# Performance work log

Hardware: AMD Instinct MI355X
Metric: run time of the kernel (lower is better)

## Reference

```python
import jax, jax.numpy as jnp
import numpy as np

N, E = 50000, 800000
IN_CH, OUT_CH = 128, 16
H1, D1 = 2, 2 * OUT_CH           # conv1: heads=2, per-head dim 32, concat -> 64
MID = H1 * D1                    # 64
NEG_SLOPE = 0.2

def setup_inputs() -> dict:
    key = jax.random.key(0)
    ks = jax.random.split(key, 16)
    s = lambda k, shape: jax.random.normal(k, shape, dtype=jnp.float32) * 0.1
    return {
        "x": jax.random.normal(ks[0], (N, IN_CH), dtype=jnp.float32),
        "edge_index": jax.random.randint(ks[1], (2, E), 0, N, dtype=jnp.int64),
        "W1": s(ks[2], (IN_CH, H1 * D1)),
        "att_src1": s(ks[3], (H1, D1)),
        "att_dst1": s(ks[4], (H1, D1)),
        "b1": jnp.zeros((MID,), jnp.float32),
        "W_mu": s(ks[5], (MID, OUT_CH)),
        "att_src_mu": s(ks[6], (1, OUT_CH)),
        "att_dst_mu": s(ks[7], (1, OUT_CH)),
        "b_mu": jnp.zeros((OUT_CH,), jnp.float32),
        "W_ls": s(ks[8], (MID, OUT_CH)),
        "att_src_ls": s(ks[9], (1, OUT_CH)),
        "att_dst_ls": s(ks[10], (1, OUT_CH)),
        "b_ls": jnp.zeros((OUT_CH,), jnp.float32),
    }

def gat_conv(x, src, dst, W, att_src, att_dst, bias, heads, d):
    # x: [N, F]; src/dst: [E'] (self loops included); PyG GATConv, eval mode (dropout off)
    n = x.shape[0]
    h = (x @ W).reshape(n, heads, d)                     # [N, H, D]
    a_src = jnp.sum(h * att_src, axis=-1)                # [N, H]
    a_dst = jnp.sum(h * att_dst, axis=-1)                # [N, H]
    e = jax.nn.leaky_relu(a_src[src] + a_dst[dst], NEG_SLOPE)   # [E', H]
    # segment softmax over incoming edges of each destination node
    m = jax.ops.segment_max(e, dst, num_segments=n)
    ex = jnp.exp(e - m[dst])
    denom = jax.ops.segment_sum(ex, dst, num_segments=n)
    alpha = ex / (denom[dst] + 1e-16)                    # [E', H]
    msg = h[src] * alpha[:, :, None]                     # [E', H, D]
    out = jax.ops.segment_sum(msg, dst, num_segments=n)  # [N, H, D]
    return out, bias

def reference(x, edge_index, W1, att_src1, att_dst1, b1,
              W_mu, att_src_mu, att_dst_mu, b_mu,
              W_ls, att_src_ls, att_dst_ls, b_ls):
    n = x.shape[0]
    loops = jnp.arange(n, dtype=edge_index.dtype)
    src = jnp.concatenate([edge_index[0], loops])        # add_self_loops=True (inputs have none)
    dst = jnp.concatenate([edge_index[1], loops])
    h, b = gat_conv(x, src, dst, W1, att_src1, att_dst1, b1, H1, D1)
    h = jax.nn.relu(h.reshape(n, H1 * D1) + b)           # concat=True -> [N, 64]
    mu, bm = gat_conv(h, src, dst, W_mu, att_src_mu, att_dst_mu, b_mu, 1, OUT_CH)
    ls, bl = gat_conv(h, src, dst, W_ls, att_src_ls, att_dst_ls, b_ls, 1, OUT_CH)
    mu = mu.mean(axis=1) + bm                            # concat=False, heads=1 -> mean == squeeze
    ls = ls.mean(axis=1) + bl
    return (mu, ls)
```

## Files before the change

### kernel.cpp

```cpp
#include <hip/hip_runtime.h>

#define NEG 0.2f

typedef __attribute__((ext_vector_type(8))) short short8;
typedef __attribute__((ext_vector_type(4))) float f32x4;

__device__ __forceinline__ float lrelu(float v) { return v > 0.f ? v : NEG * v; }

__device__ __forceinline__ unsigned short f2bf(float f) {
    unsigned u = __float_as_uint(f);
    unsigned r = (u + 0x7FFF + ((u >> 16) & 1)) >> 16;
    return (unsigned short)r;
}
__device__ __forceinline__ float bf2f(unsigned short h) { return __uint_as_float((unsigned)h << 16); }
__device__ __forceinline__ float bf_lo(unsigned v) { return __uint_as_float(v << 16); }
__device__ __forceinline__ float bf_hi(unsigned v) { return __uint_as_float(v & 0xffff0000u); }

__global__ void build_w(const float* __restrict__ W1, const float* __restrict__ as1,
                        const float* __restrict__ ad1,
                        const float* __restrict__ Wmu, const float* __restrict__ Wls,
                        const float* __restrict__ asmu, const float* __restrict__ admu,
                        const float* __restrict__ asls, const float* __restrict__ adls,
                        unsigned short* __restrict__ w1h, unsigned short* __restrict__ w1l,
                        unsigned short* __restrict__ w2h, unsigned short* __restrict__ w2l) {
    int i = blockIdx.x * blockDim.x + threadIdx.x;
    if (i < 128 * 80) {
        int k = i / 80, c = i % 80;
        float val;
        if (c < 64) val = W1[k * 64 + c];
        else if (c < 68) {
            int j = c - 64;
            int hh = j & 1;
            const float* att = (j >= 2) ? ad1 : as1;
            float s = 0.f;
            for (int d = 0; d < 32; ++d) s += W1[k * 64 + hh * 32 + d] * att[hh * 32 + d];
            val = s;
        } else val = 0.f;
        unsigned short h = f2bf(val);
        w1h[c * 128 + k] = h;
        w1l[c * 128 + k] = f2bf(val - bf2f(h));
    } else {
        int i2 = i - 128 * 80;
        if (i2 >= 64 * 48) return;
        int k = i2 / 48, c = i2 % 48;
        float val;
        if (c < 16) val = Wmu[k * 16 + c];
        else if (c < 32) val = Wls[k * 16 + (c - 16)];
        else if (c < 36) {
            int j = c - 32;
            const float* W = (j < 2) ? Wmu : Wls;
            const float* att = (j == 0) ? asmu : (j == 1) ? admu : (j == 2) ? asls : adls;
            float s = 0.f;
            for (int c2 = 0; c2 < 16; ++c2) s += W[k * 16 + c2] * att[c2];
            val = s;
        } else val = 0.f;
        unsigned short h = f2bf(val);
        w2h[c * 64 + k] = h;
        w2l[c * 64 + k] = f2bf(val - bf2f(h));
    }
}

__global__ __launch_bounds__(256) void gemm1(const float* __restrict__ x,
                                             const unsigned short* __restrict__ Wt_hi,
                                             const unsigned short* __restrict__ Wt_lo,
                                             unsigned short* __restrict__ hbf,
                                             float* __restrict__ a1, float2* __restrict__ a1s, int n) {
    int wid = threadIdx.x >> 6, lane = threadIdx.x & 63;
    int m = lane & 15, b = lane >> 4;
    int row = blockIdx.x * 64 + wid * 16 + m;
    int rowc = min(row, n - 1);
    short8 ah[4], al[4];
    const float* xp = x + (size_t)rowc * 128 + b * 8;
#pragma unroll
    for (int kc = 0; kc < 4; ++kc) {
        float4 v0 = *(const float4*)(xp + kc * 32);
        float4 v1 = *(const float4*)(xp + kc * 32 + 4);
        float vv[8] = {v0.x, v0.y, v0.z, v0.w, v1.x, v1.y, v1.z, v1.w};
#pragma unroll
        for (int j = 0; j < 8; ++j) {
            unsigned short h = f2bf(vv[j]);
            ah[kc][j] = (short)h;
            al[kc][j] = (short)f2bf(vv[j] - bf2f(h));
        }
    }
    int orow0 = blockIdx.x * 64 + wid * 16 + b * 4;
#pragma unroll
    for (int ct = 0; ct < 5; ++ct) {
        f32x4 acc = {0.f, 0.f, 0.f, 0.f};
        int col = ct * 16 + m;
        const unsigned short* wh = Wt_hi + col * 128 + b * 8;
        const unsigned short* wl = Wt_lo + col * 128 + b * 8;
#pragma unroll
        for (int kc = 0; kc < 4; ++kc) {
            short8 bh = *(const short8*)(wh + kc * 32);
            short8 bl = *(const short8*)(wl + kc * 32);
            acc = __builtin_amdgcn_mfma_f32_16x16x32_bf16(ah[kc], bh, acc, 0, 0, 0);
            acc = __builtin_amdgcn_mfma_f32_16x16x32_bf16(al[kc], bh, acc, 0, 0, 0);
            acc = __builtin_amdgcn_mfma_f32_16x16x32_bf16(ah[kc], bl, acc, 0, 0, 0);
        }
        if (ct < 4) {
#pragma unroll
            for (int j = 0; j < 4; ++j) {
                int orow = orow0 + j;
                if (orow < n) hbf[(size_t)orow * 64 + ct * 16 + m] = f2bf(acc[j]);
            }
        } else {
            int base = lane & 48;
#pragma unroll
            for (int j = 0; j < 4; ++j) {
                float c0 = __shfl(acc[j], base + 0, 64);
                float c1 = __shfl(acc[j], base + 1, 64);
                int orow = orow0 + j;
                if (orow < n) {
                    if (m < 4) a1[(size_t)orow * 4 + m] = acc[j];
                    if (m == 0) a1s[orow] = make_float2(c0, c1);
                }
            }
        }
    }
}

__global__ __launch_bounds__(256) void gemm2(const unsigned short* __restrict__ h1bf,
                                             const unsigned short* __restrict__ Wt_hi,
                                             const unsigned short* __restrict__ Wt_lo,
                                             unsigned* __restrict__ hml, float* __restrict__ a2,
                                             float2* __restrict__ a2s, int n) {
    int wid = threadIdx.x >> 6, lane = threadIdx.x & 63;
    int m = lane & 15, b = lane >> 4;
    int row = blockIdx.x * 64 + wid * 16 + m;
    int rowc = min(row, n - 1);
    short8 a0 = *(const short8*)(h1bf + (size_t)rowc * 64 + b * 8);
    short8 a1f = *(const short8*)(h1bf + (size_t)rowc * 64 + 32 + b * 8);
    int orow0 = blockIdx.x * 64 + wid * 16 + b * 4;
    f32x4 accs[3];
#pragma unroll
    for (int ct = 0; ct < 3; ++ct) {
        f32x4 acc = {0.f, 0.f, 0.f, 0.f};
        int col = ct * 16 + m;
        const unsigned short* wh = Wt_hi + col * 64 + b * 8;
        const unsigned short* wl = Wt_lo + col * 64 + b * 8;
        short8 bh0 = *(const short8*)(wh);
        short8 bl0 = *(const short8*)(wl);
        short8 bh1 = *(const short8*)(wh + 32);
        short8 bl1 = *(const short8*)(wl + 32);
        acc = __builtin_amdgcn_mfma_f32_16x16x32_bf16(a0, bh0, acc, 0, 0, 0);
        acc = __builtin_amdgcn_mfma_f32_16x16x32_bf16(a0, bl0, acc, 0, 0, 0);
        acc = __builtin_amdgcn_mfma_f32_16x16x32_bf16(a1f, bh1, acc, 0, 0, 0);
        acc = __builtin_amdgcn_mfma_f32_16x16x32_bf16(a1f, bl1, acc, 0, 0, 0);
        accs[ct] = acc;
    }
    int base = lane & 48;
#pragma unroll
    for (int j = 0; j < 4; ++j) {
        int orow = orow0 + j;
        float c0 = __shfl(accs[2][j], base + 0, 64);
        float c2 = __shfl(accs[2][j], base + 2, 64);
        if (orow >= n) continue;
        hml[(size_t)orow * 16 + m] = ((unsigned)f2bf(accs[1][j]) << 16) | f2bf(accs[0][j]);
        if (m < 4) a2[(size_t)orow * 4 + m] = accs[2][j];
        if (m == 0) a2s[orow] = make_float2(c0, c2);
    }
}

__global__ __launch_bounds__(256) void count_deg_part(const int* __restrict__ dstv, int E, int np,
                                                      int* __restrict__ deg) {
    int p = blockIdx.x & 7;
    int bslot = blockIdx.x >> 3;
    int nblk = gridDim.x >> 3;
    int lo = p * np, hi = lo + np;
    for (int i = bslot * 256 + threadIdx.x; i < E; i += nblk * 256) {
        int d = dstv[i];
        if (d >= lo && d < hi) atomicAdd(&deg[d], 1);
    }
}

__global__ __launch_bounds__(256) void scatter_part(const int* __restrict__ srcv,
                                                    const int* __restrict__ dstv, int E, int np,
                                                    int* __restrict__ cursor, int* __restrict__ srcs) {
    int p = blockIdx.x & 7;
    int bslot = blockIdx.x >> 3;
    int nblk = gridDim.x >> 3;
    int lo = p * np, hi = lo + np;
    for (int i = bslot * 256 + threadIdx.x; i < E; i += nblk * 256) {
        int d = dstv[i];
        if (d >= lo && d < hi) {
            int slot = atomicAdd(&cursor[d], 1);
            srcs[slot] = srcv[i];
        }
    }
}

__global__ __launch_bounds__(256) void block_sums(const int* __restrict__ deg, int n,
                                                  int* __restrict__ bsums) {
    int i = blockIdx.x * 256 + threadIdx.x;
    int v = (i < n) ? deg[i] : 0;
    for (int o = 32; o > 0; o >>= 1) v += __shfl_down(v, o, 64);
    __shared__ int ws[4];
    if ((threadIdx.x & 63) == 0) ws[threadIdx.x >> 6] = v;
    __syncthreads();
    if (threadIdx.x == 0) bsums[blockIdx.x] = ws[0] + ws[1] + ws[2] + ws[3];
}

__global__ __launch_bounds__(256) void write_offs(const int* __restrict__ deg,
                                                  const int* __restrict__ bsums, int nb, int n,
                                                  int* __restrict__ offs, int* __restrict__ cursor) {
    __shared__ int sb[256];
    __shared__ int s[256];
    int t = threadIdx.x;
    int bv = (t < nb) ? bsums[t] : 0;
    sb[t] = bv;
    __syncthreads();
    for (int o = 1; o < 256; o <<= 1) {
        int u = (t >= o) ? sb[t - o] : 0;
        __syncthreads();
        sb[t] += u;
        __syncthreads();
    }
    int base0 = (blockIdx.x == 0) ? 0 : sb[blockIdx.x - 1];
    int i = blockIdx.x * 256 + t;
    int v = (i < n) ? deg[i] : 0;
    s[t] = v;
    __syncthreads();
    for (int o = 1; o < 256; o <<= 1) {
        int u = (t >= o) ? s[t - o] : 0;
        __syncthreads();
        s[t] += u;
        __syncthreads();
    }
    int excl = s[t] - v + base0;
    if (i < n) { offs[i] = excl; cursor[i] = excl; }
    if (i == n - 1) offs[n] = excl + v;
}

__global__ __launch_bounds__(256) void agg1(const unsigned* __restrict__ h32, const float* __restrict__ a1,
                                            const float2* __restrict__ a1s,
                                            const int* __restrict__ offs, const int* __restrict__ srcs,
                                            const float* __restrict__ b1, unsigned* __restrict__ h1u, int n) {
    int wid = threadIdx.x >> 6, lane = threadIdx.x & 63;
    int node = blockIdx.x * 4 + wid;
    if (node >= n) return;
    int q = lane >> 4;
    int l = lane & 15;
    int head = l >> 3;
    float adst = a1[node * 4 + 2 + head];
    float ax = 0.f, ay = 0.f, az = 0.f, aw = 0.f, denom = 0.f;
    if (q == 0) {
        float w = __expf(lrelu(a1[node * 4 + head] + adst));
        uint2 hv = *(const uint2*)&h32[node * 32 + 2 * l];
        ax = w * bf_lo(hv.x); ay = w * bf_hi(hv.x);
        az = w * bf_lo(hv.y); aw = w * bf_hi(hv.y);
        denom = w;
    }
    int kb = offs[node];
    int deg = offs[node + 1] - kb;
    int pre = (lane < deg) ? srcs[kb + lane] : 0;
    for (int idx0 = 0; idx0 < deg; idx0 += 4) {
        int idx = idx0 + q;
        int idc = min(idx, deg - 1);
        int s = (idc < 64) ? __shfl(pre, idc, 64) : srcs[kb + idc];
        float2 ap = a1s[s];
        float asrc = head ? ap.y : ap.x;
        float wv = (idx < deg) ? __expf(lrelu(asrc + adst)) : 0.f;
        uint2 hv = *(const uint2*)&h32[s * 32 + 2 * l];
        denom += wv;
        ax += wv * bf_lo(hv.x); ay += wv * bf_hi(hv.x);
        az += wv * bf_lo(hv.y); aw += wv * bf_hi(hv.y);
    }
    ax += __shfl_xor(ax, 16, 64); ax += __shfl_xor(ax, 32, 64);
    ay += __shfl_xor(ay, 16, 64); ay += __shfl_xor(ay, 32, 64);
    az += __shfl_xor(az, 16, 64); az += __shfl_xor(az, 32, 64);
    aw += __shfl_xor(aw, 16, 64); aw += __shfl_xor(aw, 32, 64);
    denom += __shfl_xor(denom, 16, 64); denom += __shfl_xor(denom, 32, 64);
    if (q == 0) {
        float4 bv = *(const float4*)&b1[4 * l];
        float o0 = fmaxf(ax / denom + bv.x, 0.f);
        float o1 = fmaxf(ay / denom + bv.y, 0.f);
        float o2 = fmaxf(az / denom + bv.z, 0.f);
        float o3 = fmaxf(aw / denom + bv.w, 0.f);
        uint2 o;
        o.x = ((unsigned)f2bf(o1) << 16) | f2bf(o0);
        o.y = ((unsigned)f2bf(o3) << 16) | f2bf(o2);
        *(uint2*)&h1u[node * 32 + 2 * l] = o;
    }
}

__global__ __launch_bounds__(256) void agg2(const unsigned* __restrict__ hml,
                                            const float* __restrict__ a2, const float2* __restrict__ a2s,
                                            const int* __restrict__ offs, const int* __restrict__ srcs,
                                            const float* __restrict__ bmu, const float* __restrict__ bls,
                                            float* __restrict__ out, int n) {
    int wid = threadIdx.x >> 6, lane = threadIdx.x & 63;
    int node = blockIdx.x * 4 + wid;
    if (node >= n) return;
    int q = lane >> 4, c = lane & 15;
    float admu = a2[node * 4 + 1], adls = a2[node * 4 + 3];
    float amu = 0.f, als = 0.f, dmu = 0.f, dls = 0.f;
    if (q == 0) {
        float wmu = __expf(lrelu(a2[node * 4 + 0] + admu));
        float wls = __expf(lrelu(a2[node * 4 + 2] + adls));
        unsigned hv = hml[node * 16 + c];
        amu = wmu * bf_lo(hv); als = wls * bf_hi(hv);
        dmu = wmu; dls = wls;
    }
    int kb = offs[node];
    int deg = offs[node + 1] - kb;
    int pre = (lane < deg) ? srcs[kb + lane] : 0;
    for (int idx0 = 0; idx0 < deg; idx0 += 4) {
        int idx = idx0 + q;
        int idc = min(idx, deg - 1);
        int s = (idc < 64) ? __shfl(pre, idc, 64) : srcs[kb + idc];
        float2 ap = a2s[s];
        bool ok = idx < deg;
        float w1v = ok ? __expf(lrelu(ap.x + admu)) : 0.f;
        float w2v = ok ? __expf(lrelu(ap.y + adls)) : 0.f;
        unsigned hv = hml[s * 16 + c];
        dmu += w1v; dls += w2v;
        amu += w1v * bf_lo(hv);
        als += w2v * bf_hi(hv);
    }
    amu += __shfl_xor(amu, 16, 64); amu += __shfl_xor(amu, 32, 64);
    als += __shfl_xor(als, 16, 64); als += __shfl_xor(als, 32, 64);
    dmu += __shfl_xor(dmu, 16, 64); dmu += __shfl_xor(dmu, 32, 64);
    dls += __shfl_xor(dls, 16, 64); dls += __shfl_xor(dls, 32, 64);
    if (q == 0) {
        out[node * 16 + c] = amu / dmu + bmu[c];
        out[(size_t)n * 16 + node * 16 + c] = als / dls + bls[c];
    }
}

extern "C" void kernel_launch(void* const* d_in, const int* in_sizes, int n_in,
                              void* d_out, int out_size, void* d_ws, size_t ws_size,
                              hipStream_t stream) {
    const float* x    = (const float*)d_in[0];
    const int*   ei   = (const int*)d_in[1];
    const float* W1   = (const float*)d_in[2];
    const float* as1  = (const float*)d_in[3];
    const float* ad1  = (const float*)d_in[4];
    const float* b1   = (const float*)d_in[5];
    const float* Wmu  = (const float*)d_in[6];
    const float* asmu = (const float*)d_in[7];
    const float* admu = (const float*)d_in[8];
    const float* bmu  = (const float*)d_in[9];
    const float* Wls  = (const float*)d_in[10];
    const float* asls = (const float*)d_in[11];
    const float* adls = (const float*)d_in[12];
    const float* bls  = (const float*)d_in[13];
    float* out = (float*)d_out;

    int n = in_sizes[0] / 128;
    int E = in_sizes[1] / 2;
    int np = (n + 7) / 8;

    char* ws = (char*)d_ws;
    size_t off = 0;
    auto alloc = [&](size_t b) { size_t p = off; off = (off + b + 255) & ~(size_t)255; return p; };

    unsigned short* hbf  = (unsigned short*)(ws + alloc((size_t)n * 64 * 2));
    unsigned*       h1u  = (unsigned*)(ws + alloc((size_t)n * 32 * 4));
    float*          a1   = (float*)(ws + alloc((size_t)n * 4 * 4));
    float2*         a1s  = (float2*)(ws + alloc((size_t)n * 8));
    unsigned*       hml  = (unsigned*)(ws + alloc((size_t)n * 16 * 4));
    float*          a2   = (float*)(ws + alloc((size_t)n * 4 * 4));
    float2*         a2s  = (float2*)(ws + alloc((size_t)n * 8));
    unsigned short* w1h  = (unsigned short*)(ws + alloc(80 * 128 * 2));
    unsigned short* w1l  = (unsigned short*)(ws + alloc(80 * 128 * 2));
    unsigned short* w2h  = (unsigned short*)(ws + alloc(48 * 64 * 2));
    unsigned short* w2l  = (unsigned short*)(ws + alloc(48 * 64 * 2));
    int*   deg    = (int*)(ws + alloc((size_t)n * 4));
    int*   offs   = (int*)(ws + alloc((size_t)(n + 1) * 4));
    int*   cursor = (int*)(ws + alloc((size_t)n * 4));
    int*   srcs   = (int*)(ws + alloc((size_t)E * 4));
    int*   bsums  = (int*)(ws + alloc(1024 * 4));

    int nb = (n + 255) / 256;

    hipMemsetAsync(deg, 0, (size_t)n * 4, stream);
    build_w<<<(128 * 80 + 64 * 48 + 255) / 256, 256, 0, stream>>>(W1, as1, ad1, Wmu, Wls, asmu, admu,
                                                                  asls, adls, w1h, w1l, w2h, w2l);
    gemm1<<<(n + 63) / 64, 256, 0, stream>>>(x, w1h, w1l, hbf, a1, a1s, n);
    count_deg_part<<<2048, 256, 0, stream>>>(ei + E, E, np, deg);
    block_sums<<<nb, 256, 0, stream>>>(deg, n, bsums);
    write_offs<<<nb, 256, 0, stream>>>(deg, bsums, nb, n, offs, cursor);
    scatter_part<<<2048, 256, 0, stream>>>(ei, ei + E, E, np, cursor, srcs);
    agg1<<<(n + 3) / 4, 256, 0, stream>>>((const unsigned*)hbf, a1, a1s, offs, srcs, b1, h1u, n);
    gemm2<<<(n + 63) / 64, 256, 0, stream>>>((const unsigned short*)h1u, w2h, w2l, hml, a2, a2s, n);
    agg2<<<(n + 3) / 4, 256, 0, stream>>>(hml, a2, a2s, offs, srcs, bmu, bls, out, n);
}
```

Measured before the change: 284.2 us.

## Pre-bin edges by destination partition before degree counting and CSR scatter

Adds a bin_edges pass that buckets (src,dst) pairs into 8 destination partitions using a shared-memory histogram. Degree counting and scatter then read only their own partition instead of each of 8 block groups scanning and filtering the whole edge list. The aggregation loops also drop the shuffle-based prefetch of source indices and load srcs directly with a strided loop. This costs an extra pairs buffer and one pass writing 8-byte pairs, and relies on each partition's count staying under a fixed capacity (E/8+8192), which could overflow on skewed graphs.

```diff
diff --git a/kernel.cpp b/kernel.cpp
--- a/kernel.cpp
+++ b/kernel.cpp
@@ -162,31 +162,56 @@
     }
 }
 
-__global__ __launch_bounds__(256) void count_deg_part(const int* __restrict__ dstv, int E, int np,
-                                                      int* __restrict__ deg) {
+__global__ __launch_bounds__(256) void bin_edges(const int* __restrict__ srcv,
+                                                 const int* __restrict__ dstv, int E, int np, int cap,
+                                                 int* __restrict__ pcnt, int2* __restrict__ pairs) {
+    __shared__ int hist[8], base[8], cur[8];
+    int t = threadIdx.x;
+    if (t < 8) { hist[t] = 0; cur[t] = 0; }
+    __syncthreads();
+    int e0 = blockIdx.x * 1024;
+    int e1 = min(e0 + 1024, E);
+    int d[4], se[4];
+    int cnt = 0;
+    for (int e = e0 + t; e < e1; e += 256) {
+        int dd = dstv[e];
+        d[cnt] = dd; se[cnt] = e; ++cnt;
+        atomicAdd(&hist[(unsigned)dd / (unsigned)np], 1);
+    }
+    __syncthreads();
+    if (t < 8) base[t] = atomicAdd(&pcnt[t], hist[t]);
+    __syncthreads();
+    for (int j = 0; j < cnt; ++j) {
+        int p = (unsigned)d[j] / (unsigned)np;
+        int slot = atomicAdd(&cur[p], 1);
+        pairs[(size_t)p * cap + base[p] + slot] = make_int2(srcv[se[j]], d[j]);
+    }
+}
+
+__global__ __launch_bounds__(256) void count_pairs(const int2* __restrict__ pairs,
+                                                   const int* __restrict__ pcnt, int cap,
+                                                   int* __restrict__ deg) {
     int p = blockIdx.x & 7;
     int bslot = blockIdx.x >> 3;
     int nblk = gridDim.x >> 3;
-    int lo = p * np, hi = lo + np;
-    for (int i = bslot * 256 + threadIdx.x; i < E; i += nblk * 256) {
-        int d = dstv[i];
-        if (d >= lo && d < hi) atomicAdd(&deg[d], 1);
-    }
-}
-
-__global__ __launch_bounds__(256) void scatter_part(const int* __restrict__ srcv,
-                                                    const int* __restrict__ dstv, int E, int np,
-                                                    int* __restrict__ cursor, int* __restrict__ srcs) {
+    int cnt = pcnt[p];
+    const int2* pp = pairs + (size_t)p * cap;
+    for (int i = bslot * 256 + threadIdx.x; i < cnt; i += nblk * 256)
+        atomicAdd(&deg[pp[i].y], 1);
+}
+
+__global__ __launch_bounds__(256) void scatter_pairs(const int2* __restrict__ pairs,
+                                                     const int* __restrict__ pcnt, int cap,
+                                                     int* __restrict__ cursor, int* __restrict__ srcs) {
     int p = blockIdx.x & 7;
     int bslot = blockIdx.x >> 3;
     int nblk = gridDim.x >> 3;
-    int lo = p * np, hi = lo + np;
-    for (int i = bslot * 256 + threadIdx.x; i < E; i += nblk * 256) {
-        int d = dstv[i];
-        if (d >= lo && d < hi) {
-            int slot = atomicAdd(&cursor[d], 1);
-            srcs[slot] = srcv[i];
-        }
+    int cnt = pcnt[p];
+    const int2* pp = pairs + (size_t)p * cap;
+    for (int i = bslot * 256 + threadIdx.x; i < cnt; i += nblk * 256) {
+        int2 e = pp[i];
+        int slot = atomicAdd(&cursor[e.y], 1);
+        srcs[slot] = e.x;
     }
 }
 
@@ -251,16 +276,12 @@
         az = w * bf_lo(hv.y); aw = w * bf_hi(hv.y);
         denom = w;
     }
-    int kb = offs[node];
-    int deg = offs[node + 1] - kb;
-    int pre = (lane < deg) ? srcs[kb + lane] : 0;
-    for (int idx0 = 0; idx0 < deg; idx0 += 4) {
-        int idx = idx0 + q;
-        int idc = min(idx, deg - 1);
-        int s = (idc < 64) ? __shfl(pre, idc, 64) : srcs[kb + idc];
+    int kb = offs[node], ke = offs[node + 1];
+    for (int k = kb + q; k < ke; k += 4) {
+        int s = srcs[k];
         float2 ap = a1s[s];
         float asrc = head ? ap.y : ap.x;
-        float wv = (idx < deg) ? __expf(lrelu(asrc + adst)) : 0.f;
+        float wv = __expf(lrelu(asrc + adst));
         uint2 hv = *(const uint2*)&h32[s * 32 + 2 * l];
         denom += wv;
         ax += wv * bf_lo(hv.x); ay += wv * bf_hi(hv.x);
@@ -302,17 +323,12 @@
         amu = wmu * bf_lo(hv); als = wls * bf_hi(hv);
         dmu = wmu; dls = wls;
     }
-    int kb = offs[node];
-    int deg = offs[node + 1] - kb;
-    int pre = (lane < deg) ? srcs[kb + lane] : 0;
-    for (int idx0 = 0; idx0 < deg; idx0 += 4) {
-        int idx = idx0 + q;
-        int idc = min(idx, deg - 1);
-        int s = (idc < 64) ? __shfl(pre, idc, 64) : srcs[kb + idc];
+    int kb = offs[node], ke = offs[node + 1];
+    for (int k = kb + q; k < ke; k += 4) {
+        int s = srcs[k];
         float2 ap = a2s[s];
-        bool ok = idx < deg;
-        float w1v = ok ? __expf(lrelu(ap.x + admu)) : 0.f;
-        float w2v = ok ? __expf(lrelu(ap.y + adls)) : 0.f;
+        float w1v = __expf(lrelu(ap.x + admu));
+        float w2v = __expf(lrelu(ap.y + adls));
         unsigned hv = hml[s * 16 + c];
         dmu += w1v; dls += w2v;
         amu += w1v * bf_lo(hv);
@@ -350,6 +366,7 @@
     int n = in_sizes[0] / 128;
     int E = in_sizes[1] / 2;
     int np = (n + 7) / 8;
+    int cap = E / 8 + 8192;
 
     char* ws = (char*)d_ws;
     size_t off = 0;
@@ -366,22 +383,26 @@
     unsigned short* w1l  = (unsigned short*)(ws + alloc(80 * 128 * 2));
     unsigned short* w2h  = (unsigned short*)(ws + alloc(48 * 64 * 2));
     unsigned short* w2l  = (unsigned short*)(ws + alloc(48 * 64 * 2));
-    int*   deg    = (int*)(ws + alloc((size_t)n * 4));
+    int*   deg    = (int*)(ws + alloc((size_t)(n + 8) * 4));
+    int*   pcnt   = deg + n;
     int*   offs   = (int*)(ws + alloc((size_t)(n + 1) * 4));
     int*   cursor = (int*)(ws + alloc((size_t)n * 4));
     int*   srcs   = (int*)(ws + alloc((size_t)E * 4));
     int*   bsums  = (int*)(ws + alloc(1024 * 4));
+    int2*  pairs  = (int2*)(ws + alloc((size_t)8 * cap * 8));
 
     int nb = (n + 255) / 256;
-
-    hipMemsetAsync(deg, 0, (size_t)n * 4, stream);
+    int nbin = (E + 1023) / 1024;
+
+    hipMemsetAsync(deg, 0, (size_t)(n + 8) * 4, stream);
     build_w<<<(128 * 80 + 64 * 48 + 255) / 256, 256, 0, stream>>>(W1, as1, ad1, Wmu, Wls, asmu, admu,
                                                                   asls, adls, w1h, w1l, w2h, w2l);
     gemm1<<<(n + 63) / 64, 256, 0, stream>>>(x, w1h, w1l, hbf, a1, a1s, n);
-    count_deg_part<<<2048, 256, 0, stream>>>(ei + E, E, np, deg);
+    bin_edges<<<nbin, 256, 0, stream>>>(ei, ei + E, E, np, cap, pcnt, pairs);
+    count_pairs<<<2048, 256, 0, stream>>>(pairs, pcnt, cap, deg);
     block_sums<<<nb, 256, 0, stream>>>(deg, n, bsums);
     write_offs<<<nb, 256, 0, stream>>>(deg, bsums, nb, n, offs, cursor);
-    scatter_part<<<2048, 256, 0, stream>>>(ei, ei + E, E, np, cursor, srcs);
+    scatter_pairs<<<2048, 256, 0, stream>>>(pairs, pcnt, cap, cursor, srcs);
     agg1<<<(n + 3) / 4, 256, 0, stream>>>((const unsigned*)hbf, a1, a1s, offs, srcs, b1, h1u, n);
     gemm2<<<(n + 63) / 64, 256, 0, stream>>>((const unsigned short*)h1u, w2h, w2l, hml, a2, a2s, n);
     agg2<<<(n + 3) / 4, 256, 0, stream>>>(hml, a2, a2s, offs, srcs, bmu, bls, out, n);
```

Result: no change. 285.3 us (+0.4%).

## Fuse layer-2 projection GEMM into first aggregation kernel and unroll edge loops

Applied to the files above, without the earlier changes.

Removes the separate gemm2 launch and the h1 intermediate buffer by computing the 64x36 second-layer projection (mu, logstd and attention scores) inside the first aggregation kernel, in fp32 from shared memory. Each 4-node block now loads the full 36x64 weight matrix into LDS and does a small scalar matvec, which adds per-block overhead and two barriers. Separately, both aggregation loops drop the lane-shuffle source prefetch and process two edges per iteration so more loads are in flight.

```diff
diff --git a/kernel.cpp b/kernel.cpp
--- a/kernel.cpp
+++ b/kernel.cpp
@@ -22,7 +22,7 @@
                         const float* __restrict__ asmu, const float* __restrict__ admu,
                         const float* __restrict__ asls, const float* __restrict__ adls,
                         unsigned short* __restrict__ w1h, unsigned short* __restrict__ w1l,
-                        unsigned short* __restrict__ w2h, unsigned short* __restrict__ w2l) {
+                        float* __restrict__ w2f) {
     int i = blockIdx.x * blockDim.x + threadIdx.x;
     if (i < 128 * 80) {
         int k = i / 80, c = i % 80;
@@ -41,22 +41,20 @@
         w1l[c * 128 + k] = f2bf(val - bf2f(h));
     } else {
         int i2 = i - 128 * 80;
-        if (i2 >= 64 * 48) return;
-        int k = i2 / 48, c = i2 % 48;
+        if (i2 >= 64 * 36) return;
+        int k = i2 / 36, c = i2 % 36;
         float val;
         if (c < 16) val = Wmu[k * 16 + c];
         else if (c < 32) val = Wls[k * 16 + (c - 16)];
-        else if (c < 36) {
+        else {
             int j = c - 32;
             const float* W = (j < 2) ? Wmu : Wls;
             const float* att = (j == 0) ? asmu : (j == 1) ? admu : (j == 2) ? asls : adls;
             float s = 0.f;
             for (int c2 = 0; c2 < 16; ++c2) s += W[k * 16 + c2] * att[c2];
             val = s;
-        } else val = 0.f;
-        unsigned short h = f2bf(val);
-        w2h[c * 64 + k] = h;
-        w2l[c * 64 + k] = f2bf(val - bf2f(h));
+        }
+        w2f[c * 64 + k] = val;
     }
 }
 
@@ -117,48 +115,6 @@
                 }
             }
         }
-    }
-}
-
-__global__ __launch_bounds__(256) void gemm2(const unsigned short* __restrict__ h1bf,
-                                             const unsigned short* __restrict__ Wt_hi,
-                                             const unsigned short* __restrict__ Wt_lo,
-                                             unsigned* __restrict__ hml, float* __restrict__ a2,
-                                             float2* __restrict__ a2s, int n) {
-    int wid = threadIdx.x >> 6, lane = threadIdx.x & 63;
-    int m = lane & 15, b = lane >> 4;
-    int row = blockIdx.x * 64 + wid * 16 + m;
-    int rowc = min(row, n - 1);
-    short8 a0 = *(const short8*)(h1bf + (size_t)rowc * 64 + b * 8);
-    short8 a1f = *(const short8*)(h1bf + (size_t)rowc * 64 + 32 + b * 8);
-    int orow0 = blockIdx.x * 64 + wid * 16 + b * 4;
-    f32x4 accs[3];
-#pragma unroll
-    for (int ct = 0; ct < 3; ++ct) {
-        f32x4 acc = {0.f, 0.f, 0.f, 0.f};
-        int col = ct * 16 + m;
-        const unsigned short* wh = Wt_hi + col * 64 + b * 8;
-        const unsigned short* wl = Wt_lo + col * 64 + b * 8;
-        short8 bh0 = *(const short8*)(wh);
-        short8 bl0 = *(const short8*)(wl);
-        short8 bh1 = *(const short8*)(wh + 32);
-        short8 bl1 = *(const short8*)(wl + 32);
-        acc = __builtin_amdgcn_mfma_f32_16x16x32_bf16(a0, bh0, acc, 0, 0, 0);
-        acc = __builtin_amdgcn_mfma_f32_16x16x32_bf16(a0, bl0, acc, 0, 0, 0);
-        acc = __builtin_amdgcn_mfma_f32_16x16x32_bf16(a1f, bh1, acc, 0, 0, 0);
-        acc = __builtin_amdgcn_mfma_f32_16x16x32_bf16(a1f, bl1, acc, 0, 0, 0);
-        accs[ct] = acc;
-    }
-    int base = lane & 48;
-#pragma unroll
-    for (int j = 0; j < 4; ++j) {
-        int orow = orow0 + j;
-        float c0 = __shfl(accs[2][j], base + 0, 64);
-        float c2 = __shfl(accs[2][j], base + 2, 64);
-        if (orow >= n) continue;
-        hml[(size_t)orow * 16 + m] = ((unsigned)f2bf(accs[1][j]) << 16) | f2bf(accs[0][j]);
-        if (m < 4) a2[(size_t)orow * 4 + m] = accs[2][j];
-        if (m == 0) a2s[orow] = make_float2(c0, c2);
     }
 }
 
@@ -232,39 +188,60 @@
     if (i == n - 1) offs[n] = excl + v;
 }
 
-__global__ __launch_bounds__(256) void agg1(const unsigned* __restrict__ h32, const float* __restrict__ a1,
-                                            const float2* __restrict__ a1s,
-                                            const int* __restrict__ offs, const int* __restrict__ srcs,
-                                            const float* __restrict__ b1, unsigned* __restrict__ h1u, int n) {
-    int wid = threadIdx.x >> 6, lane = threadIdx.x & 63;
+__global__ __launch_bounds__(256) void agg1f(const unsigned* __restrict__ h32, const float* __restrict__ a1,
+                                             const float2* __restrict__ a1s,
+                                             const int* __restrict__ offs, const int* __restrict__ srcs,
+                                             const float* __restrict__ b1, const float* __restrict__ w2f,
+                                             unsigned* __restrict__ hml, float* __restrict__ a2,
+                                             float2* __restrict__ a2s, int n) {
+    __shared__ float ws2[36 * 65];
+    __shared__ float h1s[4][68];
+    __shared__ float vout[4][36];
+    int t = threadIdx.x;
+    for (int i = t; i < 36 * 64; i += 256) {
+        int c = i >> 6, k = i & 63;
+        ws2[c * 65 + k] = w2f[i];
+    }
+    int wid = t >> 6, lane = t & 63;
     int node = blockIdx.x * 4 + wid;
-    if (node >= n) return;
+    int nodec = min(node, n - 1);
     int q = lane >> 4;
     int l = lane & 15;
     int head = l >> 3;
-    float adst = a1[node * 4 + 2 + head];
+    float adst = a1[nodec * 4 + 2 + head];
     float ax = 0.f, ay = 0.f, az = 0.f, aw = 0.f, denom = 0.f;
     if (q == 0) {
-        float w = __expf(lrelu(a1[node * 4 + head] + adst));
-        uint2 hv = *(const uint2*)&h32[node * 32 + 2 * l];
+        float w = __expf(lrelu(a1[nodec * 4 + head] + adst));
+        uint2 hv = *(const uint2*)&h32[nodec * 32 + 2 * l];
         ax = w * bf_lo(hv.x); ay = w * bf_hi(hv.x);
         az = w * bf_lo(hv.y); aw = w * bf_hi(hv.y);
         denom = w;
     }
-    int kb = offs[node];
-    int deg = offs[node + 1] - kb;
-    int pre = (lane < deg) ? srcs[kb + lane] : 0;
-    for (int idx0 = 0; idx0 < deg; idx0 += 4) {
-        int idx = idx0 + q;
-        int idc = min(idx, deg - 1);
-        int s = (idc < 64) ? __shfl(pre, idc, 64) : srcs[kb + idc];
-        float2 ap = a1s[s];
-        float asrc = head ? ap.y : ap.x;
-        float wv = (idx < deg) ? __expf(lrelu(asrc + adst)) : 0.f;
-        uint2 hv = *(const uint2*)&h32[s * 32 + 2 * l];
-        denom += wv;
-        ax += wv * bf_lo(hv.x); ay += wv * bf_hi(hv.x);
-        az += wv * bf_lo(hv.y); aw += wv * bf_hi(hv.y);
+    int kb = offs[nodec], ke = offs[nodec + 1];
+    int k = kb + q;
+    while (k + 4 < ke) {
+        int s0 = srcs[k], s1 = srcs[k + 4];
+        float2 ap0 = a1s[s0];
+        float2 ap1 = a1s[s1];
+        uint2 hv0 = *(const uint2*)&h32[s0 * 32 + 2 * l];
+        uint2 hv1 = *(const uint2*)&h32[s1 * 32 + 2 * l];
+        float w0 = __expf(lrelu((head ? ap0.y : ap0.x) + adst));
+        float w1 = __expf(lrelu((head ? ap1.y : ap1.x) + adst));
+        denom += w0 + w1;
+        ax += w0 * bf_lo(hv0.x) + w1 * bf_lo(hv1.x);
+        ay += w0 * bf_hi(hv0.x) + w1 * bf_hi(hv1.x);
+        az += w0 * bf_lo(hv0.y) + w1 * bf_lo(hv1.y);
+        aw += w0 * bf_hi(hv0.y) + w1 * bf_hi(hv1.y);
+        k += 8;
+    }
+    if (k < ke) {
+        int s0 = srcs[k];
+        float2 ap0 = a1s[s0];
+        uint2 hv0 = *(const uint2*)&h32[s0 * 32 + 2 * l];
+        float w0 = __expf(lrelu((head ? ap0.y : ap0.x) + adst));
+        denom += w0;
+        ax += w0 * bf_lo(hv0.x); ay += w0 * bf_hi(hv0.x);
+        az += w0 * bf_lo(hv0.y); aw += w0 * bf_hi(hv0.y);
     }
     ax += __shfl_xor(ax, 16, 64); ax += __shfl_xor(ax, 32, 64);
     ay += __shfl_xor(ay, 16, 64); ay += __shfl_xor(ay, 32, 64);
@@ -273,14 +250,33 @@
     denom += __shfl_xor(denom, 16, 64); denom += __shfl_xor(denom, 32, 64);
     if (q == 0) {
         float4 bv = *(const float4*)&b1[4 * l];
-        float o0 = fmaxf(ax / denom + bv.x, 0.f);
-        float o1 = fmaxf(ay / denom + bv.y, 0.f);
-        float o2 = fmaxf(az / denom + bv.z, 0.f);
-        float o3 = fmaxf(aw / denom + bv.w, 0.f);
-        uint2 o;
-        o.x = ((unsigned)f2bf(o1) << 16) | f2bf(o0);
-        o.y = ((unsigned)f2bf(o3) << 16) | f2bf(o2);
-        *(uint2*)&h1u[node * 32 + 2 * l] = o;
+        float4 o;
+        o.x = fmaxf(ax / denom + bv.x, 0.f);
+        o.y = fmaxf(ay / denom + bv.y, 0.f);
+        o.z = fmaxf(az / denom + bv.z, 0.f);
+        o.w = fmaxf(aw / denom + bv.w, 0.f);
+        *(float4*)&h1s[wid][4 * l] = o;
+    }
+    __syncthreads();
+    for (int o = t; o < 144; o += 256) {
+        int nd = o / 36, col = o % 36;
+        const float* hr = h1s[nd];
+        const float* wr = &ws2[col * 65];
+        float s = 0.f;
+#pragma unroll 16
+        for (int k2 = 0; k2 < 64; ++k2) s += hr[k2] * wr[k2];
+        vout[nd][col] = s;
+    }
+    __syncthreads();
+    if (t < 64) {
+        int nd = t >> 4, c = t & 15;
+        int g = blockIdx.x * 4 + nd;
+        if (g < n) {
+            float mu = vout[nd][c], ls = vout[nd][16 + c];
+            hml[(size_t)g * 16 + c] = ((unsigned)f2bf(ls) << 16) | f2bf(mu);
+            if (c < 4) a2[(size_t)g * 4 + c] = vout[nd][32 + c];
+            if (c == 0) a2s[g] = make_float2(vout[nd][32], vout[nd][34]);
+        }
     }
 }
 
@@ -302,21 +298,32 @@
         amu = wmu * bf_lo(hv); als = wls * bf_hi(hv);
         dmu = wmu; dls = wls;
     }
-    int kb = offs[node];
-    int deg = offs[node + 1] - kb;
-    int pre = (lane < deg) ? srcs[kb + lane] : 0;
-    for (int idx0 = 0; idx0 < deg; idx0 += 4) {
-        int idx = idx0 + q;
-        int idc = min(idx, deg - 1);
-        int s = (idc < 64) ? __shfl(pre, idc, 64) : srcs[kb + idc];
-        float2 ap = a2s[s];
-        bool ok = idx < deg;
-        float w1v = ok ? __expf(lrelu(ap.x + admu)) : 0.f;
-        float w2v = ok ? __expf(lrelu(ap.y + adls)) : 0.f;
-        unsigned hv = hml[s * 16 + c];
-        dmu += w1v; dls += w2v;
-        amu += w1v * bf_lo(hv);
-        als += w2v * bf_hi(hv);
+    int kb = offs[node], ke = offs[node + 1];
+    int k = kb + q;
+    while (k + 4 < ke) {
+        int s0 = srcs[k], s1 = srcs[k + 4];
+        float2 ap0 = a2s[s0];
+        float2 ap1 = a2s[s1];
+        unsigned hv0 = hml[s0 * 16 + c];
+        unsigned hv1 = hml[s1 * 16 + c];
+        float w10 = __expf(lrelu(ap0.x + admu));
+        float w20 = __expf(lrelu(ap0.y + adls));
+        float w11 = __expf(lrelu(ap1.x + admu));
+        float w21 = __expf(lrelu(ap1.y + adls));
+        dmu += w10 + w11; dls += w20 + w21;
+        amu += w10 * bf_lo(hv0) + w11 * bf_lo(hv1);
+        als += w20 * bf_hi(hv0) + w21 * bf_hi(hv1);
+        k += 8;
+    }
+    if (k < ke) {
+        int s0 = srcs[k];
+        float2 ap0 = a2s[s0];
+        unsigned hv0 = hml[s0 * 16 + c];
+        float w10 = __expf(lrelu(ap0.x + admu));
+        float w20 = __expf(lrelu(ap0.y + adls));
+        dmu += w10; dls += w20;
+        amu += w10 * bf_lo(hv0);
+        als += w20 * bf_hi(hv0);
     }
     amu += __shfl_xor(amu, 16, 64); amu += __shfl_xor(amu, 32, 64);
     als += __shfl_xor(als, 16, 64); als += __shfl_xor(als, 32, 64);
@@ -356,7 +363,6 @@
     auto alloc = [&](size_t b) { size_t p = off; off = (off + b + 255) & ~(size_t)255; return p; };
 
     unsigned short* hbf  = (unsigned short*)(ws + alloc((size_t)n * 64 * 2));
-    unsigned*       h1u  = (unsigned*)(ws + alloc((size_t)n * 32 * 4));
     float*          a1   = (float*)(ws + alloc((size_t)n * 4 * 4));
     float2*         a1s  = (float2*)(ws + alloc((size_t)n * 8));
     unsigned*       hml  = (unsigned*)(ws + alloc((size_t)n * 16 * 4));
@@ -364,8 +370,7 @@
     float2*         a2s  = (float2*)(ws + alloc((size_t)n * 8));
     unsigned short* w1h  = (unsigned short*)(ws + alloc(80 * 128 * 2));
     unsigned short* w1l  = (unsigned short*)(ws + alloc(80 * 128 * 2));
-    unsigned short* w2h  = (unsigned short*)(ws + alloc(48 * 64 * 2));
-    unsigned short* w2l  = (unsigned short*)(ws + alloc(48 * 64 * 2));
+    float*          w2f  = (float*)(ws + alloc(36 * 64 * 4));
     int*   deg    = (int*)(ws + alloc((size_t)n * 4));
     int*   offs   = (int*)(ws + alloc((size_t)(n + 1) * 4));
     int*   cursor = (int*)(ws + alloc((size_t)n * 4));
@@ -375,14 +380,14 @@
     int nb = (n + 255) / 256;
 
     hipMemsetAsync(deg, 0, (size_t)n * 4, stream);
-    build_w<<<(128 * 80 + 64 * 48 + 255) / 256, 256, 0, stream>>>(W1, as1, ad1, Wmu, Wls, asmu, admu,
-                                                                  asls, adls, w1h, w1l, w2h, w2l);
+    build_w<<<(128 * 80 + 64 * 36 + 255) / 256, 256, 0, stream>>>(W1, as1, ad1, Wmu, Wls, asmu, admu,
+                                                                  asls, adls, w1h, w1l, w2f);
     gemm1<<<(n + 63) / 64, 256, 0, stream>>>(x, w1h, w1l, hbf, a1, a1s, n);
     count_deg_part<<<2048, 256, 0, stream>>>(ei + E, E, np, deg);
     block_sums<<<nb, 256, 0, stream>>>(deg, n, bsums);
     write_offs<<<nb, 256, 0, stream>>>(deg, bsums, nb, n, offs, cursor);
     scatter_part<<<2048, 256, 0, stream>>>(ei, ei + E, E, np, cursor, srcs);
-    agg1<<<(n + 3) / 4, 256, 0, stream>>>((const unsigned*)hbf, a1, a1s, offs, srcs, b1, h1u, n);
-    gemm2<<<(n + 63) / 64, 256, 0, stream>>>((const unsigned short*)h1u, w2h, w2l, hml, a2, a2s, n);
+    agg1f<<<(n + 3) / 4, 256, 0, stream>>>((const unsigned*)hbf, a1, a1s, offs, srcs, b1, w2f,
+                                           hml, a2, a2s, n);
     agg2<<<(n + 3) / 4, 256, 0, stream>>>(hml, a2, a2s, offs, srcs, bmu, bls, out, n);
 }
```

Measured after the change: 285.3 us. No clear change (+0.4%).
